# Optimization experiments

Measured on AMD Instinct MI355X. Metric: run time of the kernel, lower is better.

The kernel has to match this reference:

```python
import jax, jax.numpy as jnp
import numpy as np


def setup_inputs() -> dict:
    key = jax.random.key(0)
    kq, kk, kv = jax.random.split(key, 3)
    B, H, S, D = 4, 16, 2048, 64
    q = jax.random.normal(kq, (B, H, S, D), dtype=jnp.float32)
    k = jax.random.normal(kk, (B, H, S, D), dtype=jnp.float32)
    v = jax.random.normal(kv, (B, H, S, D), dtype=jnp.float32)
    return {"q": q, "k": k, "v": v}


def reference(q, k, v):
    # scale = sqrt(d_k); source's self.scale is undefined, standard SDPA scaling assumed
    scale = jnp.asarray(np.sqrt(q.shape[-1]), dtype=q.dtype)
    # [B,H,S,S] scores; sigmoid instead of softmax (no normalization across keys)
    scores = jnp.einsum("bhqd,bhkd->bhqk", q, k) / scale
    attn = jax.nn.sigmoid(scores)
    return jnp.einsum("bhqk,bhkd->bhqd", attn, v)
```

## Files before the change

### kernel.cpp

```cpp
#include <hip/hip_runtime.h>


typedef __bf16 bf16_t;
typedef __attribute__((ext_vector_type(8))) __bf16 bf16x8;
typedef __attribute__((ext_vector_type(4))) __bf16 bf16x4;
typedef __attribute__((ext_vector_type(4))) float  f32x4;

#if __has_builtin(__builtin_amdgcn_exp2f)
#define FAST_EXP2(x) __builtin_amdgcn_exp2f(x)
#else
#define FAST_EXP2(x) exp2f(x)
#endif
#if __has_builtin(__builtin_amdgcn_rcpf)
#define FAST_RCP(x) __builtin_amdgcn_rcpf(x)
#else
#define FAST_RCP(x) (1.0f / (x))
#endif

static constexpr int SEQ = 2048;
static constexpr int DH  = 64;
static constexpr int KB  = 32;
static constexpr int NIT = SEQ / KB;
static constexpr int QPW = 64;
static constexpr int QPB = 256;

__global__ __launch_bounds__(256, 2)
void sigattn_kernel(const float* __restrict__ Qg, const float* __restrict__ Kg,
                    const float* __restrict__ Vg, float* __restrict__ Og)
{
    __shared__ bf16_t Kbuf[2][4 * 64 * 8];
    __shared__ bf16_t Vbuf[2][4 * 64 * 8];
    __shared__ bf16_t Pbuf[4][QPW * KB];

    const int t    = threadIdx.x;
    const int wave = t >> 6;
    const int lane = t & 63;
    const int c16  = lane & 15;
    const int g4   = lane >> 4;

    const int bh    = blockIdx.x;
    const int qtile = blockIdx.y;

    const size_t hbase = (size_t)bh * SEQ * DH;
    const float* Qp = Qg + hbase;
    const float* Kp = Kg + hbase;
    const float* Vp = Vg + hbase;
    float*       Op = Og + hbase;

    const int qwave = qtile * QPB + wave * QPW;

    const float qscale = -0.125f * 1.44269504088896340736f;
    bf16x8 qf[4][2];
    #pragma unroll
    for (int qs = 0; qs < 4; ++qs) {
        #pragma unroll
        for (int dh = 0; dh < 2; ++dh) {
            const float* p = Qp + (size_t)(qwave + qs * 16 + c16) * DH + dh * 32 + g4 * 8;
            f32x4 a = *(const f32x4*)p;
            f32x4 b = *(const f32x4*)(p + 4);
            bf16x8 f;
            f[0] = (bf16_t)(a.x * qscale); f[1] = (bf16_t)(a.y * qscale);
            f[2] = (bf16_t)(a.z * qscale); f[3] = (bf16_t)(a.w * qscale);
            f[4] = (bf16_t)(b.x * qscale); f[5] = (bf16_t)(b.y * qscale);
            f[6] = (bf16_t)(b.z * qscale); f[7] = (bf16_t)(b.w * qscale);
            qf[qs][dh] = f;
        }
    }

    const int sks = wave >> 1;
    const int sdh = wave & 1;

    f32x4 kst0, kst1;
    float vst[8];
    auto issue_loads = [&](int kb0) {
        const float* pk = Kp + (size_t)(kb0 + sks * 16 + c16) * DH + sdh * 32 + g4 * 8;
        kst0 = *(const f32x4*)pk;
        kst1 = *(const f32x4*)(pk + 4);
        const float* pv = Vp + (size_t)(kb0 + g4 * 8) * DH + wave * 16 + c16;
        #pragma unroll
        for (int j = 0; j < 8; ++j) vst[j] = pv[(size_t)j * DH];
    };
    auto store_lds = [&](int buf) {
        bf16x8 k8;
        k8[0] = (bf16_t)kst0.x; k8[1] = (bf16_t)kst0.y; k8[2] = (bf16_t)kst0.z; k8[3] = (bf16_t)kst0.w;
        k8[4] = (bf16_t)kst1.x; k8[5] = (bf16_t)kst1.y; k8[6] = (bf16_t)kst1.z; k8[7] = (bf16_t)kst1.w;
        *(bf16x8*)&Kbuf[buf][t * 8] = k8;
        bf16x8 v8;
        #pragma unroll
        for (int j = 0; j < 8; ++j) v8[j] = (bf16_t)vst[j];
        *(bf16x8*)&Vbuf[buf][t * 8] = v8;
    };

    issue_loads(0);
    store_lds(0);

    f32x4 acc[4][4] = {};

    for (int it = 0; it < NIT; ++it) {
        const int buf = it & 1;
        __syncthreads();
        if (it + 1 < NIT) issue_loads((it + 1) * KB);

        bf16x8 kf[4], vf[4];
        #pragma unroll
        for (int f = 0; f < 4; ++f) kf[f] = *(const bf16x8*)&Kbuf[buf][(f * 64 + lane) * 8];
        #pragma unroll
        for (int f = 0; f < 4; ++f) vf[f] = *(const bf16x8*)&Vbuf[buf][(f * 64 + lane) * 8];

        #pragma unroll
        for (int qs = 0; qs < 4; ++qs) {
            #pragma unroll
            for (int ks = 0; ks < 2; ++ks) {
                f32x4 s = {0.f, 0.f, 0.f, 0.f};
                s = __builtin_amdgcn_mfma_f32_16x16x32_bf16(kf[ks * 2 + 0], qf[qs][0], s, 0, 0, 0);
                s = __builtin_amdgcn_mfma_f32_16x16x32_bf16(kf[ks * 2 + 1], qf[qs][1], s, 0, 0, 0);
                bf16x4 p4;
                #pragma unroll
                for (int r = 0; r < 4; ++r)
                    p4[r] = (bf16_t)FAST_RCP(1.0f + FAST_EXP2(s[r]));
                *(bf16x4*)&Pbuf[wave][(qs * 64 + (ks * 2 + (g4 >> 1)) * 16 + c16) * 8 + (g4 & 1) * 4] = p4;
            }
        }

        asm volatile("s_waitcnt lgkmcnt(0)" ::: "memory");

        #pragma unroll
        for (int qs = 0; qs < 4; ++qs) {
            bf16x8 pf = *(const bf16x8*)&Pbuf[wave][(qs * 64 + lane) * 8];
            #pragma unroll
            for (int dt = 0; dt < 4; ++dt)
                acc[qs][dt] = __builtin_amdgcn_mfma_f32_16x16x32_bf16(pf, vf[dt], acc[qs][dt], 0, 0, 0);
        }

        if (it + 1 < NIT) store_lds(buf ^ 1);
    }

    #pragma unroll
    for (int qs = 0; qs < 4; ++qs) {
        const int q0 = qwave + qs * 16 + g4 * 4;
        #pragma unroll
        for (int r = 0; r < 4; ++r) {
            float* po = Op + (size_t)(q0 + r) * DH + c16;
            po[0]  = acc[qs][0][r];
            po[16] = acc[qs][1][r];
            po[32] = acc[qs][2][r];
            po[48] = acc[qs][3][r];
        }
    }
}

extern "C" void kernel_launch(void* const* d_in, const int* in_sizes, int n_in,
                              void* d_out, int out_size, void* d_ws, size_t ws_size,
                              hipStream_t stream)
{
    const float* q = (const float*)d_in[0];
    const float* k = (const float*)d_in[1];
    const float* v = (const float*)d_in[2];
    float* o = (float*)d_out;
    dim3 grid(64, SEQ / QPB);
    sigattn_kernel<<<grid, dim3(256), 0, stream>>>(q, k, v, o);
}
```

Before: 207.9 us.

## Feed sigmoid scores straight into PV MFMA from registers, halve per-wave query tile

The P tile no longer round-trips through LDS. The sigmoid scores in the MFMA accumulator layout are fed directly as the A operand of 16x16x16 bf16 MFMAs, and the V staging layout is remapped to match. Queries per wave drop from 64 to 32 and launch bounds go to 4 blocks per SM, which doubles the grid and targets higher occupancy. The cost is twice as many K/V tile loads per query, and PV now uses 16x16x16 MFMAs, which may have lower throughput than the 16x16x32 form.

```diff
diff --git a/kernel.cpp b/kernel.cpp
--- a/kernel.cpp
+++ b/kernel.cpp
@@ -5,32 +5,51 @@
 typedef __attribute__((ext_vector_type(8))) __bf16 bf16x8;
 typedef __attribute__((ext_vector_type(4))) __bf16 bf16x4;
 typedef __attribute__((ext_vector_type(4))) float  f32x4;
+typedef __attribute__((ext_vector_type(4))) short  short4v;
 
-#if __has_builtin(__builtin_amdgcn_exp2f)
+#if defined(__HIP_DEVICE_COMPILE__) && __has_builtin(__builtin_amdgcn_exp2f)
 #define FAST_EXP2(x) __builtin_amdgcn_exp2f(x)
 #else
 #define FAST_EXP2(x) exp2f(x)
 #endif
-#if __has_builtin(__builtin_amdgcn_rcpf)
+#if defined(__HIP_DEVICE_COMPILE__) && __has_builtin(__builtin_amdgcn_rcpf)
 #define FAST_RCP(x) __builtin_amdgcn_rcpf(x)
 #else
 #define FAST_RCP(x) (1.0f / (x))
 #endif
 
+static __device__ __forceinline__ f32x4 pv_mfma(bf16x4 a, bf16x4 b, f32x4 c) {
+#if defined(__HIP_DEVICE_COMPILE__)
+#if __has_builtin(__builtin_amdgcn_mfma_f32_16x16x16_bf16)
+    return __builtin_amdgcn_mfma_f32_16x16x16_bf16(a, b, c, 0, 0, 0);
+#elif __has_builtin(__builtin_amdgcn_mfma_f32_16x16x16bf16_1k)
+    return __builtin_amdgcn_mfma_f32_16x16x16bf16_1k(
+        __builtin_bit_cast(short4v, a), __builtin_bit_cast(short4v, b), c, 0, 0, 0);
+#else
+    f32x4 d;
+    asm("v_mfma_f32_16x16x16_bf16 %0, %1, %2, %3"
+        : "=v"(d) : "v"(a), "v"(b), "v"(c));
+    return d;
+#endif
+#else
+    (void)a; (void)b;
+    return c;
+#endif
+}
+
 static constexpr int SEQ = 2048;
 static constexpr int DH  = 64;
 static constexpr int KB  = 32;
 static constexpr int NIT = SEQ / KB;
-static constexpr int QPW = 64;
-static constexpr int QPB = 256;
+static constexpr int QPW = 32;
+static constexpr int QPB = 128;
 
-__global__ __launch_bounds__(256, 2)
+__global__ __launch_bounds__(256, 4)
 void sigattn_kernel(const float* __restrict__ Qg, const float* __restrict__ Kg,
                     const float* __restrict__ Vg, float* __restrict__ Og)
 {
     __shared__ bf16_t Kbuf[2][4 * 64 * 8];
     __shared__ bf16_t Vbuf[2][4 * 64 * 8];
-    __shared__ bf16_t Pbuf[4][QPW * KB];
 
     const int t    = threadIdx.x;
     const int wave = t >> 6;
@@ -50,9 +69,9 @@
     const int qwave = qtile * QPB + wave * QPW;
 
     const float qscale = -0.125f * 1.44269504088896340736f;
-    bf16x8 qf[4][2];
+    bf16x8 qf[2][2];
     #pragma unroll
-    for (int qs = 0; qs < 4; ++qs) {
+    for (int qs = 0; qs < 2; ++qs) {
         #pragma unroll
         for (int dh = 0; dh < 2; ++dh) {
             const float* p = Qp + (size_t)(qwave + qs * 16 + c16) * DH + dh * 32 + g4 * 8;
@@ -67,18 +86,18 @@
         }
     }
 
-    const int sks = wave >> 1;
-    const int sdh = wave & 1;
-
     f32x4 kst0, kst1;
     float vst[8];
     auto issue_loads = [&](int kb0) {
-        const float* pk = Kp + (size_t)(kb0 + sks * 16 + c16) * DH + sdh * 32 + g4 * 8;
+        const float* pk = Kp + (size_t)(kb0 + (wave >> 1) * 16 + c16) * DH + (wave & 1) * 32 + g4 * 8;
         kst0 = *(const f32x4*)pk;
         kst1 = *(const f32x4*)(pk + 4);
-        const float* pv = Vp + (size_t)(kb0 + g4 * 8) * DH + wave * 16 + c16;
+        const float* pv = Vp + (size_t)(kb0 + g4 * 4) * DH + wave * 16 + c16;
         #pragma unroll
-        for (int j = 0; j < 8; ++j) vst[j] = pv[(size_t)j * DH];
+        for (int h = 0; h < 2; ++h)
+            #pragma unroll
+            for (int j = 0; j < 4; ++j)
+                vst[h * 4 + j] = pv[(size_t)(h * 16 + j) * DH];
     };
     auto store_lds = [&](int buf) {
         bf16x8 k8;
@@ -94,7 +113,7 @@
     issue_loads(0);
     store_lds(0);
 
-    f32x4 acc[4][4] = {};
+    f32x4 acc[2][4] = {};
 
     for (int it = 0; it < NIT; ++it) {
         const int buf = it & 1;
@@ -108,35 +127,31 @@
         for (int f = 0; f < 4; ++f) vf[f] = *(const bf16x8*)&Vbuf[buf][(f * 64 + lane) * 8];
 
         #pragma unroll
-        for (int qs = 0; qs < 4; ++qs) {
+        for (int qs = 0; qs < 2; ++qs) {
             #pragma unroll
             for (int ks = 0; ks < 2; ++ks) {
                 f32x4 s = {0.f, 0.f, 0.f, 0.f};
                 s = __builtin_amdgcn_mfma_f32_16x16x32_bf16(kf[ks * 2 + 0], qf[qs][0], s, 0, 0, 0);
                 s = __builtin_amdgcn_mfma_f32_16x16x32_bf16(kf[ks * 2 + 1], qf[qs][1], s, 0, 0, 0);
-                bf16x4 p4;
+                bf16x4 p;
                 #pragma unroll
                 for (int r = 0; r < 4; ++r)
-                    p4[r] = (bf16_t)FAST_RCP(1.0f + FAST_EXP2(s[r]));
-                *(bf16x4*)&Pbuf[wave][(qs * 64 + (ks * 2 + (g4 >> 1)) * 16 + c16) * 8 + (g4 & 1) * 4] = p4;
+                    p[r] = (bf16_t)FAST_RCP(1.0f + FAST_EXP2(s[r]));
+                #pragma unroll
+                for (int dt = 0; dt < 4; ++dt) {
+                    bf16x4 vb = ks == 0
+                        ? __builtin_shufflevector(vf[dt], vf[dt], 0, 1, 2, 3)
+                        : __builtin_shufflevector(vf[dt], vf[dt], 4, 5, 6, 7);
+                    acc[qs][dt] = pv_mfma(p, vb, acc[qs][dt]);
+                }
             }
-        }
-
-        asm volatile("s_waitcnt lgkmcnt(0)" ::: "memory");
-
-        #pragma unroll
-        for (int qs = 0; qs < 4; ++qs) {
-            bf16x8 pf = *(const bf16x8*)&Pbuf[wave][(qs * 64 + lane) * 8];
-            #pragma unroll
-            for (int dt = 0; dt < 4; ++dt)
-                acc[qs][dt] = __builtin_amdgcn_mfma_f32_16x16x32_bf16(pf, vf[dt], acc[qs][dt], 0, 0, 0);
         }
 
         if (it + 1 < NIT) store_lds(buf ^ 1);
     }
 
     #pragma unroll
-    for (int qs = 0; qs < 4; ++qs) {
+    for (int qs = 0; qs < 2; ++qs) {
         const int q0 = qwave + qs * 16 + g4 * 4;
         #pragma unroll
         for (int r = 0; r < 4; ++r) {
```

New measurement: 216.5 us. +4.1%, slower.
